# Kernel tuning notes

Measured on AMD Instinct MI355X. Metric: run time of the kernel, lower is better.

Reference implementation:

```python
import jax, jax.numpy as jnp
import numpy as np
from jax import lax

# flat indices of the 8 'donut' taps in a 3x3 kernel (center position 4 stays zero),
# matching torch.nonzero row-major ordering of the mask
_DONUT_IDX = jnp.array([0, 1, 2, 3, 5, 6, 7, 8])

def _gelu(x):
    return jax.nn.gelu(x, approximate=False)  # torch nn.GELU default (erf)

def _conv(x, w, dil=1, pad=0):
    return lax.conv_general_dilated(x, w, (1, 1), [(pad, pad), (pad, pad)],
                                    rhs_dilation=(dil, dil),
                                    dimension_numbers=('NCHW', 'OIHW', 'NCHW'))

def _donut_conv(x, p, dil):
    # ParamConv_reg_variable_dilation with shuffle_true=0: scatter 8 params into a
    # 3x3 kernel (zero center) and conv with rhs_dilation=dil, padding=dil ('same').
    O, I, _ = p.shape
    k = jnp.zeros((O, I, 9), p.dtype).at[:, :, _DONUT_IDX].set(p).reshape(O, I, 3, 3)
    return _conv(x, k, dil=dil, pad=dil)

def _resblock(x, w1, w2):
    # gelu(Sequential(conv3x3, gelu, conv3x3)(x) + x)
    return _gelu(_conv(_gelu(_conv(x, w1, pad=1)), w2, pad=1) + x)

def _avgpool2(x):
    N, C, H, W = x.shape
    return x.reshape(N, C, H // 2, 2, W // 2, 2).mean(axis=(3, 5))

def _upsample(x, scale, w):
    # nn.Upsample(scale, bilinear, align_corners=False) -> half-pixel bilinear resize
    N, C, H, W = x.shape
    if scale > 1:
        x = jax.image.resize(x, (N, C, H * scale, W * scale), method='bilinear')
    return _gelu(_conv(x, w))  # 1x1 conv + gelu

def _shine_fwd(input_image, conv0a_w, conv0b_w, first_p, cl10_w, cl2_w,
               dil_p, dilres_p, ups_w, out1_w, out2_w, last_w):
    # n_frames=5, center frame index 2; H,W divisible by 64 so no pad branch
    target = input_image[:, 2:3]
    feats = jnp.concatenate([input_image[:, :2], input_image[:, 3:]], axis=1)  # [N,4,H,W]
    target = _gelu(_conv(target, conv0b_w))            # 1x1 -> 48 ch
    feats = _gelu(_conv(feats, conv0a_w, pad=1))       # 3x3 -> 16 ch
    base = jnp.concatenate([target, feats], axis=1)    # 64 ch

    outs = [_gelu(_donut_conv(base, first_p, 1))]      # first_output (dil 1)
    base = _resblock(base, cl10_w[0, 0], cl10_w[0, 1])
    outs.append(_gelu(_donut_conv(base, dilres_p[0], 3)))  # dilated_convs_res[0]
    base = _resblock(base, cl2_w[0, 0], cl2_w[0, 1])

    dils = (5, 8, 10, 11)     # dilated_convs effective dilations (add_dilation=0)
    dilres = (3, 6, 8, 9)     # dilated_convs_res effective dilations
    for i in range(4):
        m = _gelu(_donut_conv(base, dil_p[i], dils[i]))
        outs.append(_upsample(m, 2 ** i, ups_w[i]))
        if i < 3:
            base = _avgpool2(base)
            base = _resblock(base, cl10_w[i + 1, 0], cl10_w[i + 1, 1])
            m = _gelu(_donut_conv(base, dilres_p[i + 1], dilres[i + 1]))
            outs.append(_upsample(m, 2 ** (i + 1), ups_w[i + 1]))
            base = _resblock(base, cl2_w[i + 1, 0], cl2_w[i + 1, 1])

    out = jnp.concatenate(outs, axis=1)                # 9*64 = 576 ch
    out = _gelu(_conv(out, out1_w))                    # 1x1 576->288
    out = _gelu(_conv(out, out2_w))                    # 1x1 288->64
    return _conv(out, last_w)                          # 1x1 64->1

def setup_inputs():
    key = jax.random.key(0)
    ks = jax.random.split(key, 12)
    s = 0.05
    F = 64
    return {
        'input_image': jax.random.normal(ks[0], (2, 5, 256, 256), jnp.float32),
        'conv0a_w': jax.random.normal(ks[1], (16, 4, 3, 3), jnp.float32) * s,
        'conv0b_w': jax.random.normal(ks[2], (48, 1, 1, 1), jnp.float32) * s,
        'first_p': jax.random.normal(ks[3], (F, F, 8), jnp.float32) * s,
        'cl10_w': jax.random.normal(ks[4], (4, 2, F, F, 3, 3), jnp.float32) * s,
        'cl2_w': jax.random.normal(ks[5], (4, 2, F, F, 3, 3), jnp.float32) * s,
        'dil_p': jax.random.normal(ks[6], (4, F, F, 8), jnp.float32) * s,
        'dilres_p': jax.random.normal(ks[7], (4, F, F, 8), jnp.float32) * s,
        'ups_w': jax.random.normal(ks[8], (4, F, F, 1, 1), jnp.float32) * s,
        'out1_w': jax.random.normal(ks[9], (288, 576, 1, 1), jnp.float32) * s,
        'out2_w': jax.random.normal(ks[10], (64, 288, 1, 1), jnp.float32) * s,
        'last_w': jax.random.normal(ks[11], (1, 64, 1, 1), jnp.float32) * s,
    }

def reference(input_image, conv0a_w, conv0b_w, first_p, cl10_w, cl2_w,
              dil_p, dilres_p, ups_w, out1_w, out2_w, last_w):
    return _shine_fwd(input_image, conv0a_w, conv0b_w, first_p, cl10_w, cl2_w,
                      dil_p, dilres_p, ups_w, out1_w, out2_w, last_w)
```

## Files before the change

### kernel.cpp

```cpp
#include <hip/hip_runtime.h>
#include <hip/hip_bf16.h>


#define HPX 65536
#define FCH 64

typedef __attribute__((ext_vector_type(8))) short  short8;
typedef __attribute__((ext_vector_type(4))) float  floatx4;

__device__ __forceinline__ float gelu_f(float x) {
  return 0.5f * x * (1.0f + erff(x * 0.70710678118654752440f));
}
__device__ __forceinline__ unsigned short f2bf(float x) {
  unsigned u = __float_as_uint(x);
  unsigned r = (u + 0x7FFFu + ((u >> 16) & 1u)) >> 16;
  return (unsigned short)r;
}
__device__ __forceinline__ float bf2f(unsigned short h) {
  return __uint_as_float(((unsigned)h) << 16);
}

__global__ __launch_bounds__(256) void conv0_nhwc_kernel(
    const float* __restrict__ img,
    const float* __restrict__ w0a,
    const float* __restrict__ w0b,
    unsigned short* __restrict__ ohi,
    unsigned short* __restrict__ olo)
{
  long t = (long)blockIdx.x * 256 + threadIdx.x;
  int c  = (int)(t & 63);
  int px = (int)((t >> 6) & (HPX - 1));
  int n  = (int)(t >> 22);
  const float* im = img + (long)n * 5 * HPX;
  float r;
  if (c < 48) {
    r = w0b[c] * im[2 * HPX + px];
  } else {
    int co = c - 48;
    int y = px >> 8, x = px & 255;
    r = 0.0f;
    const int map4[4] = {0, 1, 3, 4};
    #pragma unroll
    for (int fi = 0; fi < 4; fi++) {
      const float* imc = im + (long)map4[fi] * HPX;
      #pragma unroll
      for (int ky = 0; ky < 3; ky++) {
        int yy = y + ky - 1;
        #pragma unroll
        for (int kx = 0; kx < 3; kx++) {
          int xx = x + kx - 1;
          bool ok = ((unsigned)yy < 256u) && ((unsigned)xx < 256u);
          float v = ok ? imc[yy * 256 + xx] : 0.0f;
          r = fmaf(w0a[((co * 4 + fi) * 3 + ky) * 3 + kx], v, r);
        }
      }
    }
  }
  float v = gelu_f(r);
  unsigned short hb = f2bf(v);
  ohi[t] = hb;
  olo[t] = f2bf(v - bf2f(hb));
}

struct JobArr { int4 j[29]; };

__global__ __launch_bounds__(256) void pack_conv_kernel(
    const float* __restrict__ cl10, const float* __restrict__ cl2,
    const float* __restrict__ first_p, const float* __restrict__ dilres_p,
    const float* __restrict__ dil_p, const float* __restrict__ ups_w,
    unsigned short* __restrict__ packs, JobArr jobs)
{
  int4 jb = jobs.j[blockIdx.y];
  int ntaps = jb.z;
  int idx = blockIdx.x * 256 + threadIdx.x;
  if (idx >= ntaps * 8192) return;
  int j  = idx & 7;
  int l  = (idx >> 3) & 63;
  int s  = (idx >> 9) & 1;
  int nt = (idx >> 10) & 3;
  int kt = (idx >> 12) & 1;
  int tap = idx >> 13;
  int oc = nt * 16 + (l & 15);
  int ci = kt * 32 + (l >> 4) * 8 + j;
  const float* src;
  switch (jb.x) {
    case 0: src = cl10; break;
    case 1: src = cl2; break;
    case 2: src = first_p; break;
    case 3: src = dilres_p; break;
    case 4: src = dil_p; break;
    default: src = ups_w; break;
  }
  float w = src[jb.y + (oc * 64 + ci) * ntaps + tap];
  unsigned short hi = f2bf(w);
  unsigned short v = (s == 0) ? hi : f2bf(w - bf2f(hi));
  packs[jb.w + idx] = v;
}

__global__ __launch_bounds__(256) void pack_w1_kernel(
    const float* __restrict__ w1, unsigned short* __restrict__ w1p)
{
  int t = blockIdx.x * 256 + threadIdx.x;
  if (t >= 18 * 18 * 512) return;
  int j = t & 7, l = (t >> 3) & 63;
  int mt = (t >> 9) % 18, kt = (t >> 9) / 18;
  int oc = mt * 16 + (l & 15);
  int k  = kt * 32 + (l >> 4) * 8 + j;
  float w = w1[oc * 576 + k];
  unsigned short hi = f2bf(w);
  unsigned short lo = f2bf(w - bf2f(hi));
  long base = ((long)(kt * 18 + mt) * 2) * 512 + l * 8 + j;
  w1p[base] = hi;
  w1p[base + 512] = lo;
}
__global__ __launch_bounds__(256) void pack_w2_kernel(
    const float* __restrict__ w2, unsigned short* __restrict__ w2p)
{
  int t = blockIdx.x * 256 + threadIdx.x;
  if (t >= 9 * 4 * 512) return;
  int j = t & 7, l = (t >> 3) & 63;
  int ot = (t >> 9) % 4, kt = (t >> 9) / 4;
  int oc = ot * 16 + (l & 15);
  int k  = kt * 32 + (l >> 4) * 8 + j;
  float w = w2[oc * 288 + k];
  unsigned short hi = f2bf(w);
  unsigned short lo = f2bf(w - bf2f(hi));
  long base = ((long)(kt * 4 + ot) * 2) * 512 + l * 8 + j;
  w2p[base] = hi;
  w2p[base + 512] = lo;
}

template <int NTAPS, int MT, bool RESID, bool TO_CONCAT>
__global__ __launch_bounds__(256) void conv_pipe_kernel(
    const unsigned short* __restrict__ in_hi,
    const unsigned short* __restrict__ in_lo,
    const unsigned short* __restrict__ wp,
    const unsigned short* __restrict__ res_hi,
    const unsigned short* __restrict__ res_lo,
    unsigned short* __restrict__ out_hi,
    unsigned short* __restrict__ out_lo,
    int Hs, int logW, int dil, int ccol)
{
  __shared__ short8 wst[2][1024];
  const int tid  = threadIdx.x;
  const int lane = tid & 63;
  const int wave = tid >> 6;
  const int row  = lane & 15;
  const int g    = lane >> 4;
  const int n    = blockIdx.z;
  const int Ws   = 1 << logW;
  const int npx_in = Hs << logW;
  const int opx0 = blockIdx.x * (64 * MT) + wave * (16 * MT);

  const unsigned short* ihi = in_hi + (long)n * npx_in * 64;
  const unsigned short* ilo = in_lo + (long)n * npx_in * 64;
  const short8* wpv = (const short8*)wp;

  int ry[MT], rx[MT];
  #pragma unroll
  for (int mt = 0; mt < MT; mt++) {
    int p = opx0 + mt * 16 + row;
    ry[mt] = p >> logW;
    rx[mt] = p & (Ws - 1);
  }

  floatx4 acc[MT][4];
  #pragma unroll
  for (int mt = 0; mt < MT; mt++)
    #pragma unroll
    for (int nt = 0; nt < 4; nt++) acc[mt][nt] = (floatx4){0.f, 0.f, 0.f, 0.f};

  const short8 zz = {0, 0, 0, 0, 0, 0, 0, 0};
  short8 sreg[4];
  short8 ahA[MT][2], alA[MT][2], ahB[MT][2], alB[MT][2];

  auto stage_issue = [&](int t) {
    #pragma unroll
    for (int p = 0; p < 4; p++)
      sreg[p] = wpv[(long)t * 1024 + tid + p * 256];
  };
  auto stage_write = [&](int b) {
    #pragma unroll
    for (int p = 0; p < 4; p++)
      wst[b][tid + p * 256] = sreg[p];
  };
  auto a_load = [&](short8 (&ah)[MT][2], short8 (&al)[MT][2], int t) {
    const int kk  = (NTAPS == 9) ? t : (t < 4 ? t : t + 1);
    const int dyd = (kk / 3 - 1) * dil, dxd = (kk % 3 - 1) * dil;
    #pragma unroll
    for (int mt = 0; mt < MT; mt++) {
      int yy = ry[mt] + dyd, xx = rx[mt] + dxd;
      bool ok = ((unsigned)yy < (unsigned)Hs) && ((unsigned)xx < (unsigned)Ws);
      long base = ok ? (long)((yy << logW) + xx) * 64 : 0;
      #pragma unroll
      for (int kt = 0; kt < 2; kt++) {
        long a = base + kt * 32 + g * 8;
        short8 h = *(const short8*)(ihi + a);
        short8 l = *(const short8*)(ilo + a);
        ah[mt][kt] = ok ? h : zz;
        al[mt][kt] = ok ? l : zz;
      }
    }
  };
  auto compute = [&](int b, short8 (&ah)[MT][2], short8 (&al)[MT][2]) {
    #pragma unroll
    for (int kt = 0; kt < 2; kt++)
      #pragma unroll
      for (int nt = 0; nt < 4; nt++) {
        short8 bh = wst[b][(kt * 4 + nt) * 128 + lane];
        short8 bl = wst[b][(kt * 4 + nt) * 128 + 64 + lane];
        #pragma unroll
        for (int mt = 0; mt < MT; mt++) {
          acc[mt][nt] = __builtin_amdgcn_mfma_f32_16x16x32_bf16(ah[mt][kt], bh, acc[mt][nt], 0, 0, 0);
          acc[mt][nt] = __builtin_amdgcn_mfma_f32_16x16x32_bf16(ah[mt][kt], bl, acc[mt][nt], 0, 0, 0);
          acc[mt][nt] = __builtin_amdgcn_mfma_f32_16x16x32_bf16(al[mt][kt], bh, acc[mt][nt], 0, 0, 0);
        }
      }
  };

  stage_issue(0);
  a_load(ahA, alA, 0);
  stage_write(0);
  __syncthreads();

  #pragma unroll
  for (int tt = 0; tt < NTAPS; tt++) {
    const int b = tt & 1;
    if (tt + 1 < NTAPS) {
      stage_issue(tt + 1);
      if ((tt & 1) == 0) a_load(ahB, alB, tt + 1);
      else               a_load(ahA, alA, tt + 1);
    }
    if ((tt & 1) == 0) compute(b, ahA, alA);
    else               compute(b, ahB, alB);
    if (tt + 1 < NTAPS) {
      stage_write(b ^ 1);
      __syncthreads();
    }
  }

  #pragma unroll
  for (int mt = 0; mt < MT; mt++) {
    #pragma unroll
    for (int nt = 0; nt < 4; nt++) {
      #pragma unroll
      for (int r = 0; r < 4; r++) {
        int px = opx0 + mt * 16 + g * 4 + r;
        int oc = nt * 16 + row;
        float v = acc[mt][nt][r];
        if (RESID) {
          long ri = ((long)n * npx_in + px) * 64 + oc;
          v += bf2f(res_hi[ri]) + bf2f(res_lo[ri]);
        }
        v = gelu_f(v);
        if (TO_CONCAT) {
          out_hi[((long)n * HPX + px) * 576 + ccol + oc] = f2bf(v);
        } else {
          long oi = ((long)n * npx_in + px) * 64 + oc;
          unsigned short hb = f2bf(v);
          out_hi[oi] = hb;
          out_lo[oi] = f2bf(v - bf2f(hb));
        }
      }
    }
  }
}

template <int NTAPS, int MT, bool RESID, bool BILIN, bool TO_CONCAT>
__global__ __launch_bounds__(256) void conv_mfma_kernel(
    const unsigned short* __restrict__ in_hi,
    const unsigned short* __restrict__ in_lo,
    const unsigned short* __restrict__ wp,
    const unsigned short* __restrict__ res_hi,
    const unsigned short* __restrict__ res_lo,
    unsigned short* __restrict__ out_hi,
    unsigned short* __restrict__ out_lo,
    int Hs, int logW, int dil, int ccol)
{
  __shared__ short8 wst[1024];
  const int tid  = threadIdx.x;
  const int lane = threadIdx.x & 63;
  const int wave = threadIdx.x >> 6;
  const int row  = lane & 15;
  const int g    = lane >> 4;
  const int n    = blockIdx.z;
  const int npx_in = Hs << logW;
  const int opx0 = blockIdx.x * (64 * MT) + wave * (16 * MT);

  const unsigned short* ihi = in_hi + (long)n * npx_in * 64;
  const unsigned short* ilo = in_lo + (long)n * npx_in * 64;
  const short8* wpv = (const short8*)wp;

  int b00[MT], b01[MT], b10[MT], b11[MT];
  float bwx[MT], bwy[MT];
  #pragma unroll
  for (int mt = 0; mt < MT; mt++) {
    int p = opx0 + mt * 16 + row;
    int Y = p >> 8, X = p & 255;
    float sc = (float)Hs * (1.0f / 256.0f);
    float fy = ((float)Y + 0.5f) * sc - 0.5f;
    float fx = ((float)X + 0.5f) * sc - 0.5f;
    int y0 = (int)floorf(fy), x0 = (int)floorf(fx);
    bwy[mt] = fy - (float)y0; bwx[mt] = fx - (float)x0;
    int y0c = min(max(y0, 0), Hs - 1), y1c = min(max(y0 + 1, 0), Hs - 1);
    int x0c = min(max(x0, 0), Hs - 1), x1c = min(max(x0 + 1, 0), Hs - 1);
    b00[mt] = (y0c * Hs + x0c) * 64; b01[mt] = (y0c * Hs + x1c) * 64;
    b10[mt] = (y1c * Hs + x0c) * 64; b11[mt] = (y1c * Hs + x1c) * 64;
  }

  floatx4 acc[MT][4];
  #pragma unroll
  for (int mt = 0; mt < MT; mt++)
    #pragma unroll
    for (int nt = 0; nt < 4; nt++) acc[mt][nt] = (floatx4){0.f, 0.f, 0.f, 0.f};

  #pragma unroll
  for (int p = 0; p < 4; p++)
    wst[tid + p * 256] = wpv[tid + p * 256];
  __syncthreads();

  #pragma unroll
  for (int kt = 0; kt < 2; kt++) {
    const int ko = kt * 32 + g * 8;
    short8 ah[MT], al[MT];
    #pragma unroll
    for (int mt = 0; mt < MT; mt++) {
      short8 h00 = *(const short8*)(ihi + b00[mt] + ko);
      short8 l00 = *(const short8*)(ilo + b00[mt] + ko);
      short8 h01 = *(const short8*)(ihi + b01[mt] + ko);
      short8 l01 = *(const short8*)(ilo + b01[mt] + ko);
      short8 h10 = *(const short8*)(ihi + b10[mt] + ko);
      short8 l10 = *(const short8*)(ilo + b10[mt] + ko);
      short8 h11 = *(const short8*)(ihi + b11[mt] + ko);
      short8 l11 = *(const short8*)(ilo + b11[mt] + ko);
      short8 hh, ll;
      #pragma unroll
      for (int j = 0; j < 8; j++) {
        float v00 = bf2f((unsigned short)h00[j]) + bf2f((unsigned short)l00[j]);
        float v01 = bf2f((unsigned short)h01[j]) + bf2f((unsigned short)l01[j]);
        float v10 = bf2f((unsigned short)h10[j]) + bf2f((unsigned short)l10[j]);
        float v11 = bf2f((unsigned short)h11[j]) + bf2f((unsigned short)l11[j]);
        float v0 = v00 + bwx[mt] * (v01 - v00);
        float v1 = v10 + bwx[mt] * (v11 - v10);
        float v  = v0 + bwy[mt] * (v1 - v0);
        unsigned short hb = f2bf(v);
        hh[j] = (short)hb;
        ll[j] = (short)f2bf(v - bf2f(hb));
      }
      ah[mt] = hh; al[mt] = ll;
    }
    #pragma unroll
    for (int nt = 0; nt < 4; nt++) {
      short8 bh = wst[(kt * 4 + nt) * 2 * 64 + lane];
      short8 bl = wst[((kt * 4 + nt) * 2 + 1) * 64 + lane];
      #pragma unroll
      for (int mt = 0; mt < MT; mt++) {
        acc[mt][nt] = __builtin_amdgcn_mfma_f32_16x16x32_bf16(ah[mt], bh, acc[mt][nt], 0, 0, 0);
        acc[mt][nt] = __builtin_amdgcn_mfma_f32_16x16x32_bf16(ah[mt], bl, acc[mt][nt], 0, 0, 0);
        acc[mt][nt] = __builtin_amdgcn_mfma_f32_16x16x32_bf16(al[mt], bh, acc[mt][nt], 0, 0, 0);
      }
    }
  }

  #pragma unroll
  for (int mt = 0; mt < MT; mt++) {
    #pragma unroll
    for (int nt = 0; nt < 4; nt++) {
      #pragma unroll
      for (int r = 0; r < 4; r++) {
        int px = opx0 + mt * 16 + g * 4 + r;
        int oc = nt * 16 + row;
        float v = gelu_f(acc[mt][nt][r]);
        out_hi[((long)n * HPX + px) * 576 + ccol + oc] = f2bf(v);
      }
    }
  }
}

__global__ __launch_bounds__(256) void avgpool_nhwc_kernel(
    const unsigned short* __restrict__ ihi, const unsigned short* __restrict__ ilo,
    unsigned short* __restrict__ ohi, unsigned short* __restrict__ olo,
    int logWo)
{
  const int lognpo = 2 * logWo;
  long t = (long)blockIdx.x * 256 + threadIdx.x;
  int cg = (int)(t & 7);
  int p  = (int)((t >> 3) & ((1 << lognpo) - 1));
  int n  = (int)(t >> (3 + lognpo));
  int y = p >> logWo, x = p & ((1 << logWo) - 1);
  int Wi = 2 << logWo;
  long ib = ((long)n * (4 << lognpo) + (long)(2 * y) * Wi + 2 * x) * 64 + cg * 8;
  short8 h00 = *(const short8*)(ihi + ib);
  short8 h01 = *(const short8*)(ihi + ib + 64);
  short8 h10 = *(const short8*)(ihi + ib + (long)Wi * 64);
  short8 h11 = *(const short8*)(ihi + ib + (long)Wi * 64 + 64);
  short8 l00 = *(const short8*)(ilo + ib);
  short8 l01 = *(const short8*)(ilo + ib + 64);
  short8 l10 = *(const short8*)(ilo + ib + (long)Wi * 64);
  short8 l11 = *(const short8*)(ilo + ib + (long)Wi * 64 + 64);
  short8 oh, ol;
  #pragma unroll
  for (int j = 0; j < 8; j++) {
    float v = 0.25f * ((bf2f((unsigned short)h00[j]) + bf2f((unsigned short)l00[j])) +
                       (bf2f((unsigned short)h01[j]) + bf2f((unsigned short)l01[j])) +
                       (bf2f((unsigned short)h10[j]) + bf2f((unsigned short)l10[j])) +
                       (bf2f((unsigned short)h11[j]) + bf2f((unsigned short)l11[j])));
    unsigned short hb = f2bf(v);
    oh[j] = (short)hb;
    ol[j] = (short)f2bf(v - bf2f(hb));
  }
  long ob = (((long)n << lognpo) + p) * 64 + cg * 8;
  *(short8*)(ohi + ob) = oh;
  *(short8*)(olo + ob) = ol;
}

__global__ __launch_bounds__(256, 2) void head_mfma_kernel(
    const unsigned short* __restrict__ v,
    const unsigned short* __restrict__ w1p,
    const unsigned short* __restrict__ w2p,
    const float* __restrict__ w3,
    float* __restrict__ out)
{
  __shared__ unsigned short hs[128][296];
  const int lane = threadIdx.x & 63;
  const int wave = threadIdx.x >> 6;
  const int col  = lane & 15;
  const int g    = lane >> 4;
  const int n    = blockIdx.y;
  const int pxb  = blockIdx.x * 128;
  const unsigned short* vn = v + ((long)n * HPX + pxb + wave * 32) * 576;
  const short8* w1v = (const short8*)w1p;
  const short8* w2v = (const short8*)w2p;

  floatx4 acc[2][18];
  #pragma unroll
  for (int t = 0; t < 2; t++)
    #pragma unroll
    for (int mt = 0; mt < 18; mt++) acc[t][mt] = (floatx4){0.f, 0.f, 0.f, 0.f};

  for (int kt = 0; kt < 18; kt++) {
    const int ko = kt * 32 + g * 8;
    short8 a0 = *(const short8*)(vn + (long)col * 576 + ko);
    short8 a1 = *(const short8*)(vn + (long)(col + 16) * 576 + ko);
    #pragma unroll
    for (int mt = 0; mt < 18; mt++) {
      short8 bhi = w1v[((kt * 18 + mt) * 2 + 0) * 64 + lane];
      short8 blo = w1v[((kt * 18 + mt) * 2 + 1) * 64 + lane];
      acc[0][mt] = __builtin_amdgcn_mfma_f32_16x16x32_bf16(a0, bhi, acc[0][mt], 0, 0, 0);
      acc[0][mt] = __builtin_amdgcn_mfma_f32_16x16x32_bf16(a0, blo, acc[0][mt], 0, 0, 0);
      acc[1][mt] = __builtin_amdgcn_mfma_f32_16x16x32_bf16(a1, bhi, acc[1][mt], 0, 0, 0);
      acc[1][mt] = __builtin_amdgcn_mfma_f32_16x16x32_bf16(a1, blo, acc[1][mt], 0, 0, 0);
    }
  }
  #pragma unroll
  for (int t = 0; t < 2; t++)
    #pragma unroll
    for (int mt = 0; mt < 18; mt++)
      #pragma unroll
      for (int r = 0; r < 4; r++)
        hs[wave * 32 + t * 16 + g * 4 + r][mt * 16 + col] =
            f2bf(gelu_f(acc[t][mt][r]));
  __syncthreads();

  floatx4 acc2[2][4];
  #pragma unroll
  for (int t = 0; t < 2; t++)
    #pragma unroll
    for (int ot = 0; ot < 4; ot++) acc2[t][ot] = (floatx4){0.f, 0.f, 0.f, 0.f};

  for (int kt = 0; kt < 9; kt++) {
    short8 a[2];
    #pragma unroll
    for (int t = 0; t < 2; t++)
      a[t] = *(const short8*)&hs[wave * 32 + t * 16 + col][kt * 32 + g * 8];
    #pragma unroll
    for (int ot = 0; ot < 4; ot++) {
      short8 bhi = w2v[((kt * 4 + ot) * 2 + 0) * 64 + lane];
      short8 blo = w2v[((kt * 4 + ot) * 2 + 1) * 64 + lane];
      acc2[0][ot] = __builtin_amdgcn_mfma_f32_16x16x32_bf16(a[0], bhi, acc2[0][ot], 0, 0, 0);
      acc2[0][ot] = __builtin_amdgcn_mfma_f32_16x16x32_bf16(a[0], blo, acc2[0][ot], 0, 0, 0);
      acc2[1][ot] = __builtin_amdgcn_mfma_f32_16x16x32_bf16(a[1], bhi, acc2[1][ot], 0, 0, 0);
      acc2[1][ot] = __builtin_amdgcn_mfma_f32_16x16x32_bf16(a[1], blo, acc2[1][ot], 0, 0, 0);
    }
  }

  float w3r[4];
  #pragma unroll
  for (int ot = 0; ot < 4; ot++) w3r[ot] = w3[ot * 16 + col];
  #pragma unroll
  for (int t = 0; t < 2; t++) {
    float r[4] = {0.f, 0.f, 0.f, 0.f};
    #pragma unroll
    for (int ot = 0; ot < 4; ot++)
      #pragma unroll
      for (int rr = 0; rr < 4; rr++)
        r[rr] = fmaf(w3r[ot], gelu_f(acc2[t][ot][rr]), r[rr]);
    #pragma unroll
    for (int rr = 0; rr < 4; rr++) {
      r[rr] += __shfl_xor(r[rr], 1);
      r[rr] += __shfl_xor(r[rr], 2);
      r[rr] += __shfl_xor(r[rr], 4);
      r[rr] += __shfl_xor(r[rr], 8);
    }
    if (col == 0) {
      int px = pxb + wave * 32 + t * 16 + g * 4;
      #pragma unroll
      for (int rr = 0; rr < 4; rr++)
        out[(long)n * HPX + px + rr] = r[rr];
    }
  }
}

extern "C" void kernel_launch(void* const* d_in, const int* in_sizes, int n_in,
                              void* d_out, int out_size, void* d_ws, size_t ws_size,
                              hipStream_t stream) {
  const float* img      = (const float*)d_in[0];
  const float* w0a      = (const float*)d_in[1];
  const float* w0b      = (const float*)d_in[2];
  const float* first_p  = (const float*)d_in[3];
  const float* cl10     = (const float*)d_in[4];
  const float* cl2      = (const float*)d_in[5];
  const float* dil_p    = (const float*)d_in[6];
  const float* dilres_p = (const float*)d_in[7];
  const float* ups_w    = (const float*)d_in[8];
  const float* w1       = (const float*)d_in[9];
  const float* w2       = (const float*)d_in[10];
  const float* w3       = (const float*)d_in[11];

  const size_t CONCAT_B = 150994944ul;
  const size_t ACT_B    = 16777216ul;
  const size_t PACKS_B  = 3604480ul;
  const size_t W1P_B    = 663552ul;
  const size_t W2P_B    = 73728ul;
  const size_t NEED = CONCAT_B + 4 * ACT_B + PACKS_B + W1P_B + W2P_B;

  if (ws_size < NEED) {
    hipMemsetAsync(d_out, 0, (size_t)out_size * 4, stream);
    return;
  }

  char* wsb = (char*)d_ws;
  unsigned short* concat = (unsigned short*)wsb;
  unsigned short* Xhi = (unsigned short*)(wsb + CONCAT_B);
  unsigned short* Xlo = (unsigned short*)(wsb + CONCAT_B + ACT_B);
  unsigned short* Yhi = (unsigned short*)(wsb + CONCAT_B + 2 * ACT_B);
  unsigned short* Ylo = (unsigned short*)(wsb + CONCAT_B + 3 * ACT_B);
  unsigned short* packs = (unsigned short*)(wsb + CONCAT_B + 4 * ACT_B);
  unsigned short* w1p = (unsigned short*)(wsb + CONCAT_B + 4 * ACT_B + PACKS_B);
  unsigned short* w2p = (unsigned short*)(wsb + CONCAT_B + 4 * ACT_B + PACKS_B + W1P_B);

  auto off_cl10   = [](int c) { return (long)c * 73728; };
  auto off_cl2    = [](int c) { return 589824l + (long)c * 73728; };
  const long OFF_FIRST = 1179648;
  auto off_dilres = [](int k) { return 1245184l + (long)k * 65536; };
  auto off_dil    = [](int k) { return 1507328l + (long)k * 65536; };
  auto off_ups    = [](int k) { return 1769472l + (long)k * 8192; };

  JobArr jobs;
  for (int c = 0; c < 8; c++) jobs.j[c]     = {0, c * 36864, 9, (int)off_cl10(c)};
  for (int c = 0; c < 8; c++) jobs.j[8 + c] = {1, c * 36864, 9, (int)off_cl2(c)};
  jobs.j[16] = {2, 0, 8, (int)OFF_FIRST};
  for (int k = 0; k < 4; k++) jobs.j[17 + k] = {3, k * 32768, 8, (int)off_dilres(k)};
  for (int k = 0; k < 4; k++) jobs.j[21 + k] = {4, k * 32768, 8, (int)off_dil(k)};
  for (int k = 0; k < 4; k++) jobs.j[25 + k] = {5, k * 4096, 1, (int)off_ups(k)};
  pack_conv_kernel<<<dim3(288, 29), 256, 0, stream>>>(
      cl10, cl2, first_p, dilres_p, dil_p, ups_w, packs, jobs);
  pack_w1_kernel<<<(18 * 18 * 512 + 255) / 256, 256, 0, stream>>>(w1, w1p);
  pack_w2_kernel<<<(9 * 4 * 512 + 255) / 256, 256, 0, stream>>>(w2, w2p);

  conv0_nhwc_kernel<<<(2 * HPX * 64) / 256, 256, 0, stream>>>(img, w0a, w0b, Xhi, Xlo);

  auto conv9 = [&](const unsigned short* ih, const unsigned short* il, long wo,
                   unsigned short* oh, unsigned short* ol, int Hs, int logW) {
    int npx = Hs << logW;
    if (npx == HPX)
      conv_pipe_kernel<9, 2, false, false><<<dim3(npx / 128, 1, 2), 256, 0, stream>>>(
          ih, il, packs + wo, nullptr, nullptr, oh, ol, Hs, logW, 1, 0);
    else
      conv_pipe_kernel<9, 1, false, false><<<dim3(npx / 64, 1, 2), 256, 0, stream>>>(
          ih, il, packs + wo, nullptr, nullptr, oh, ol, Hs, logW, 1, 0);
  };
  auto conv9r = [&](const unsigned short* ih, const unsigned short* il, long wo,
                    unsigned short* rh, unsigned short* rl, int Hs, int logW) {
    int npx = Hs << logW;
    if (npx == HPX)
      conv_pipe_kernel<9, 2, true, false><<<dim3(npx / 128, 1, 2), 256, 0, stream>>>(
          ih, il, packs + wo, rh, rl, rh, rl, Hs, logW, 1, 0);
    else
      conv_pipe_kernel<9, 1, true, false><<<dim3(npx / 64, 1, 2), 256, 0, stream>>>(
          ih, il, packs + wo, rh, rl, rh, rl, Hs, logW, 1, 0);
  };
  auto donutC = [&](const unsigned short* ih, const unsigned short* il, long wo,
                    int dil, int ccol) {
    conv_pipe_kernel<8, 2, false, true><<<dim3(512, 1, 2), 256, 0, stream>>>(
        ih, il, packs + wo, nullptr, nullptr, concat, nullptr, 256, 8, dil, ccol);
  };
  auto donutA = [&](const unsigned short* ih, const unsigned short* il, long wo,
                    int dil, unsigned short* oh, unsigned short* ol, int Hs, int logW) {
    int npx = Hs << logW;
    if (npx == HPX)
      conv_pipe_kernel<8, 2, false, false><<<dim3(npx / 128, 1, 2), 256, 0, stream>>>(
          ih, il, packs + wo, nullptr, nullptr, oh, ol, Hs, logW, dil, 0);
    else
      conv_pipe_kernel<8, 1, false, false><<<dim3(npx / 64, 1, 2), 256, 0, stream>>>(
          ih, il, packs + wo, nullptr, nullptr, oh, ol, Hs, logW, dil, 0);
  };
  auto upsC = [&](const unsigned short* ih, const unsigned short* il, long wo,
                  int Hs, int logW, int ccol) {
    conv_mfma_kernel<1, 4, false, true, true><<<dim3(256, 1, 2), 256, 0, stream>>>(
        ih, il, packs + wo, nullptr, nullptr, concat, nullptr, Hs, logW, 1, ccol);
  };
  auto avgp = [&](const unsigned short* ih, const unsigned short* il,
                  unsigned short* oh, unsigned short* ol, int logWo) {
    long total = 2l * (1l << (2 * logWo)) * 8;
    avgpool_nhwc_kernel<<<(int)(total / 256), 256, 0, stream>>>(ih, il, oh, ol, logWo);
  };

  donutC(Xhi, Xlo, OFF_FIRST, 1, 0);
  conv9(Xhi, Xlo, off_cl10(0), Yhi, Ylo, 256, 8);
  conv9r(Yhi, Ylo, off_cl10(1), Xhi, Xlo, 256, 8);
  donutC(Xhi, Xlo, off_dilres(0), 3, 64);
  conv9(Xhi, Xlo, off_cl2(0), Yhi, Ylo, 256, 8);
  conv9r(Yhi, Ylo, off_cl2(1), Xhi, Xlo, 256, 8);

  donutA(Xhi, Xlo, off_dil(0), 5, Yhi, Ylo, 256, 8);
  upsC(Yhi, Ylo, off_ups(0), 256, 8, 128);
  avgp(Xhi, Xlo, Yhi, Ylo, 7);
  conv9(Yhi, Ylo, off_cl10(2), Xhi, Xlo, 128, 7);
  conv9r(Xhi, Xlo, off_cl10(3), Yhi, Ylo, 128, 7);
  donutA(Yhi, Ylo, off_dilres(1), 6, Xhi, Xlo, 128, 7);
  upsC(Xhi, Xlo, off_ups(1), 128, 7, 192);
  conv9(Yhi, Ylo, off_cl2(2), Xhi, Xlo, 128, 7);
  conv9r(Xhi, Xlo, off_cl2(3), Yhi, Ylo, 128, 7);

  donutA(Yhi, Ylo, off_dil(1), 8, Xhi, Xlo, 128, 7);
  upsC(Xhi, Xlo, off_ups(1), 128, 7, 256);
  avgp(Yhi, Ylo, Xhi, Xlo, 6);
  conv9(Xhi, Xlo, off_cl10(4), Yhi, Ylo, 64, 6);
  conv9r(Yhi, Ylo, off_cl10(5), Xhi, Xlo, 64, 6);
  donutA(Xhi, Xlo, off_dilres(2), 8, Yhi, Ylo, 64, 6);
  upsC(Yhi, Ylo, off_ups(2), 64, 6, 320);
  conv9(Xhi, Xlo, off_cl2(4), Yhi, Ylo, 64, 6);
  conv9r(Yhi, Ylo, off_cl2(5), Xhi, Xlo, 64, 6);

  donutA(Xhi, Xlo, off_dil(2), 10, Yhi, Ylo, 64, 6);
  upsC(Yhi, Ylo, off_ups(2), 64, 6, 384);
  avgp(Xhi, Xlo, Yhi, Ylo, 5);
  conv9(Yhi, Ylo, off_cl10(6), Xhi, Xlo, 32, 5);
  conv9r(Xhi, Xlo, off_cl10(7), Yhi, Ylo, 32, 5);
  donutA(Yhi, Ylo, off_dilres(3), 9, Xhi, Xlo, 32, 5);
  upsC(Xhi, Xlo, off_ups(3), 32, 5, 448);
  conv9(Yhi, Ylo, off_cl2(6), Xhi, Xlo, 32, 5);
  conv9r(Xhi, Xlo, off_cl2(7), Yhi, Ylo, 32, 5);

  donutA(Yhi, Ylo, off_dil(3), 11, Xhi, Xlo, 32, 5);
  upsC(Xhi, Xlo, off_ups(3), 32, 5, 512);

  head_mfma_kernel<<<dim3(512, 2), 256, 0, stream>>>(concat, w1p, w2p, w3,
                                                     (float*)d_out);
}
```

Baseline: 1.135 ms.

## Split head into staged out1/out2 GEMMs and coalesce conv epilogue stores via LDS

The fused head kernel, which held 18 accumulator tiles per wave and read w1 straight from global memory, is replaced by two kernels run over two pixel chunks. out1 stages each w1 k-slice in LDS, spreads the 288 output channels across waves, and writes gelu(h) to a scratch buffer. out2 then stages all of w2 in LDS and computes the 64-channel layer plus the final reduction. Separately, the conv and upsample epilogues now transpose results through per-wave LDS so global writes become 16-byte vector stores instead of scattered 2-byte stores. The intermediate h makes an extra round trip through global memory, and the scratch buffer reuses the X activation buffer.

```diff
diff --git a/kernel.cpp b/kernel.cpp
--- a/kernel.cpp
+++ b/kernel.cpp
@@ -4,6 +4,7 @@
 
 #define HPX 65536
 #define FCH 64
+#define CHPX 32768
 
 typedef __attribute__((ext_vector_type(8))) short  short8;
 typedef __attribute__((ext_vector_type(4))) float  floatx4;
@@ -141,7 +142,9 @@
     unsigned short* __restrict__ out_lo,
     int Hs, int logW, int dil, int ccol)
 {
+  constexpr int PL = TO_CONCAT ? 1 : 2;
   __shared__ short8 wst[2][1024];
+  __shared__ unsigned short tb[4][PL][16][76];
   const int tid  = threadIdx.x;
   const int lane = tid & 63;
   const int wave = tid >> 6;
@@ -241,6 +244,7 @@
 
   #pragma unroll
   for (int mt = 0; mt < MT; mt++) {
+    __builtin_amdgcn_wave_barrier();
     #pragma unroll
     for (int nt = 0; nt < 4; nt++) {
       #pragma unroll
@@ -253,31 +257,42 @@
           v += bf2f(res_hi[ri]) + bf2f(res_lo[ri]);
         }
         v = gelu_f(v);
+        unsigned short hb = f2bf(v);
+        tb[wave][0][g * 4 + r][oc] = hb;
+        if (!TO_CONCAT)
+          tb[wave][PL - 1][g * 4 + r][oc] = f2bf(v - bf2f(hb));
+      }
+    }
+    __builtin_amdgcn_wave_barrier();
+    const int pxb = opx0 + mt * 16;
+    const int pxl = lane >> 2;
+    #pragma unroll
+    for (int pl = 0; pl < PL; pl++) {
+      #pragma unroll
+      for (int it = 0; it < 2; it++) {
+        int ch = (lane & 3) + it * 4;
+        short8 v8 = *(const short8*)&tb[wave][pl][pxl][ch * 8];
         if (TO_CONCAT) {
-          out_hi[((long)n * HPX + px) * 576 + ccol + oc] = f2bf(v);
+          *(short8*)&out_hi[((long)n * HPX + pxb + pxl) * 576 + ccol + ch * 8] = v8;
         } else {
-          long oi = ((long)n * npx_in + px) * 64 + oc;
-          unsigned short hb = f2bf(v);
-          out_hi[oi] = hb;
-          out_lo[oi] = f2bf(v - bf2f(hb));
+          unsigned short* dst = pl ? out_lo : out_hi;
+          *(short8*)&dst[((long)n * npx_in + pxb + pxl) * 64 + ch * 8] = v8;
         }
       }
     }
   }
 }
 
-template <int NTAPS, int MT, bool RESID, bool BILIN, bool TO_CONCAT>
-__global__ __launch_bounds__(256) void conv_mfma_kernel(
+template <int MT>
+__global__ __launch_bounds__(256) void ups_mfma_kernel(
     const unsigned short* __restrict__ in_hi,
     const unsigned short* __restrict__ in_lo,
     const unsigned short* __restrict__ wp,
-    const unsigned short* __restrict__ res_hi,
-    const unsigned short* __restrict__ res_lo,
-    unsigned short* __restrict__ out_hi,
-    unsigned short* __restrict__ out_lo,
-    int Hs, int logW, int dil, int ccol)
+    unsigned short* __restrict__ outc,
+    int Hs, int logW, int ccol)
 {
   __shared__ short8 wst[1024];
+  __shared__ unsigned short tb[4][16][76];
   const int tid  = threadIdx.x;
   const int lane = threadIdx.x & 63;
   const int wave = threadIdx.x >> 6;
@@ -364,15 +379,20 @@
 
   #pragma unroll
   for (int mt = 0; mt < MT; mt++) {
-    #pragma unroll
-    for (int nt = 0; nt < 4; nt++) {
-      #pragma unroll
-      for (int r = 0; r < 4; r++) {
-        int px = opx0 + mt * 16 + g * 4 + r;
-        int oc = nt * 16 + row;
-        float v = gelu_f(acc[mt][nt][r]);
-        out_hi[((long)n * HPX + px) * 576 + ccol + oc] = f2bf(v);
-      }
+    __builtin_amdgcn_wave_barrier();
+    #pragma unroll
+    for (int nt = 0; nt < 4; nt++)
+      #pragma unroll
+      for (int r = 0; r < 4; r++)
+        tb[wave][g * 4 + r][nt * 16 + row] = f2bf(gelu_f(acc[mt][nt][r]));
+    __builtin_amdgcn_wave_barrier();
+    const int pxb = opx0 + mt * 16;
+    const int pxl = lane >> 2;
+    #pragma unroll
+    for (int it = 0; it < 2; it++) {
+      int ch = (lane & 3) + it * 4;
+      short8 v8 = *(const short8*)&tb[wave][pxl][ch * 8];
+      *(short8*)&outc[((long)n * HPX + pxb + pxl) * 576 + ccol + ch * 8] = v8;
     }
   }
 }
@@ -414,81 +434,130 @@
   *(short8*)(olo + ob) = ol;
 }
 
-__global__ __launch_bounds__(256, 2) void head_mfma_kernel(
+__global__ __launch_bounds__(256) void out1_gemm_kernel(
     const unsigned short* __restrict__ v,
     const unsigned short* __restrict__ w1p,
+    unsigned short* __restrict__ h,
+    int cpx)
+{
+  __shared__ short8 ws8[2400];
+  const int tid  = threadIdx.x;
+  const int lane = tid & 63;
+  const int wave = tid >> 6;
+  const int row  = lane & 15;
+  const int g    = lane >> 4;
+  const int n    = blockIdx.y;
+  const int px0  = cpx + blockIdx.x * 64;
+  const int mtb  = (wave < 2) ? wave * 5 : 10 + (wave - 2) * 4;
+  const int MTN  = (wave < 2) ? 5 : 4;
+  const short8* w1v = (const short8*)w1p;
+
+  floatx4 acc[4][5];
+  #pragma unroll
+  for (int t = 0; t < 4; t++)
+    #pragma unroll
+    for (int m = 0; m < 5; m++) acc[t][m] = (floatx4){0.f, 0.f, 0.f, 0.f};
+
+  for (int kt = 0; kt < 18; kt++) {
+    __syncthreads();
+    #pragma unroll
+    for (int p = 0; p < 9; p++)
+      ws8[tid + p * 256] = w1v[kt * 2304 + tid + p * 256];
+    __syncthreads();
+
+    short8 a[4];
+    #pragma unroll
+    for (int t = 0; t < 4; t++)
+      a[t] = *(const short8*)(v + ((long)n * HPX + px0 + t * 16 + row) * 576 +
+                              kt * 32 + g * 8);
+    #pragma unroll
+    for (int m = 0; m < 5; m++) {
+      if (m < MTN) {
+        short8 bh = ws8[((mtb + m) * 2 + 0) * 64 + lane];
+        short8 bl = ws8[((mtb + m) * 2 + 1) * 64 + lane];
+        #pragma unroll
+        for (int t = 0; t < 4; t++) {
+          acc[t][m] = __builtin_amdgcn_mfma_f32_16x16x32_bf16(a[t], bh, acc[t][m], 0, 0, 0);
+          acc[t][m] = __builtin_amdgcn_mfma_f32_16x16x32_bf16(a[t], bl, acc[t][m], 0, 0, 0);
+        }
+      }
+    }
+  }
+
+  __syncthreads();
+  unsigned short* hs2 = (unsigned short*)ws8;
+  #pragma unroll
+  for (int m = 0; m < 5; m++) {
+    if (m < MTN) {
+      #pragma unroll
+      for (int t = 0; t < 4; t++)
+        #pragma unroll
+        for (int r = 0; r < 4; r++)
+          hs2[(t * 16 + g * 4 + r) * 300 + (mtb + m) * 16 + row] =
+              f2bf(gelu_f(acc[t][m][r]));
+    }
+  }
+  __syncthreads();
+  #pragma unroll
+  for (int p = 0; p < 9; p++) {
+    int li = tid + p * 256;
+    int px = li / 36, c16 = li % 36;
+    short8 v8 = *(const short8*)&hs2[px * 300 + c16 * 8];
+    *(short8*)&h[((long)n * CHPX + (px0 - cpx) + px) * 288 + c16 * 8] = v8;
+  }
+}
+
+__global__ __launch_bounds__(256) void out2_gemm_kernel(
+    const unsigned short* __restrict__ h,
     const unsigned short* __restrict__ w2p,
     const float* __restrict__ w3,
-    float* __restrict__ out)
-{
-  __shared__ unsigned short hs[128][296];
-  const int lane = threadIdx.x & 63;
-  const int wave = threadIdx.x >> 6;
-  const int col  = lane & 15;
+    float* __restrict__ out,
+    int cpx)
+{
+  __shared__ short8 w2s[4608];
+  const int tid  = threadIdx.x;
+  const int lane = tid & 63;
+  const int wave = tid >> 6;
+  const int row  = lane & 15;
   const int g    = lane >> 4;
   const int n    = blockIdx.y;
-  const int pxb  = blockIdx.x * 128;
-  const unsigned short* vn = v + ((long)n * HPX + pxb + wave * 32) * 576;
-  const short8* w1v = (const short8*)w1p;
+  const int pxc  = blockIdx.x * 256 + wave * 64;
   const short8* w2v = (const short8*)w2p;
 
-  floatx4 acc[2][18];
-  #pragma unroll
-  for (int t = 0; t < 2; t++)
-    #pragma unroll
-    for (int mt = 0; mt < 18; mt++) acc[t][mt] = (floatx4){0.f, 0.f, 0.f, 0.f};
-
-  for (int kt = 0; kt < 18; kt++) {
-    const int ko = kt * 32 + g * 8;
-    short8 a0 = *(const short8*)(vn + (long)col * 576 + ko);
-    short8 a1 = *(const short8*)(vn + (long)(col + 16) * 576 + ko);
-    #pragma unroll
-    for (int mt = 0; mt < 18; mt++) {
-      short8 bhi = w1v[((kt * 18 + mt) * 2 + 0) * 64 + lane];
-      short8 blo = w1v[((kt * 18 + mt) * 2 + 1) * 64 + lane];
-      acc[0][mt] = __builtin_amdgcn_mfma_f32_16x16x32_bf16(a0, bhi, acc[0][mt], 0, 0, 0);
-      acc[0][mt] = __builtin_amdgcn_mfma_f32_16x16x32_bf16(a0, blo, acc[0][mt], 0, 0, 0);
-      acc[1][mt] = __builtin_amdgcn_mfma_f32_16x16x32_bf16(a1, bhi, acc[1][mt], 0, 0, 0);
-      acc[1][mt] = __builtin_amdgcn_mfma_f32_16x16x32_bf16(a1, blo, acc[1][mt], 0, 0, 0);
-    }
-  }
-  #pragma unroll
-  for (int t = 0; t < 2; t++)
-    #pragma unroll
-    for (int mt = 0; mt < 18; mt++)
-      #pragma unroll
-      for (int r = 0; r < 4; r++)
-        hs[wave * 32 + t * 16 + g * 4 + r][mt * 16 + col] =
-            f2bf(gelu_f(acc[t][mt][r]));
+  #pragma unroll
+  for (int p = 0; p < 18; p++)
+    w2s[tid + p * 256] = w2v[tid + p * 256];
   __syncthreads();
 
-  floatx4 acc2[2][4];
-  #pragma unroll
-  for (int t = 0; t < 2; t++)
+  floatx4 acc2[4][4];
+  #pragma unroll
+  for (int t = 0; t < 4; t++)
     #pragma unroll
     for (int ot = 0; ot < 4; ot++) acc2[t][ot] = (floatx4){0.f, 0.f, 0.f, 0.f};
 
   for (int kt = 0; kt < 9; kt++) {
-    short8 a[2];
-    #pragma unroll
-    for (int t = 0; t < 2; t++)
-      a[t] = *(const short8*)&hs[wave * 32 + t * 16 + col][kt * 32 + g * 8];
+    short8 a[4];
+    #pragma unroll
+    for (int t = 0; t < 4; t++)
+      a[t] = *(const short8*)&h[((long)n * CHPX + pxc + t * 16 + row) * 288 +
+                                kt * 32 + g * 8];
     #pragma unroll
     for (int ot = 0; ot < 4; ot++) {
-      short8 bhi = w2v[((kt * 4 + ot) * 2 + 0) * 64 + lane];
-      short8 blo = w2v[((kt * 4 + ot) * 2 + 1) * 64 + lane];
-      acc2[0][ot] = __builtin_amdgcn_mfma_f32_16x16x32_bf16(a[0], bhi, acc2[0][ot], 0, 0, 0);
-      acc2[0][ot] = __builtin_amdgcn_mfma_f32_16x16x32_bf16(a[0], blo, acc2[0][ot], 0, 0, 0);
-      acc2[1][ot] = __builtin_amdgcn_mfma_f32_16x16x32_bf16(a[1], bhi, acc2[1][ot], 0, 0, 0);
-      acc2[1][ot] = __builtin_amdgcn_mfma_f32_16x16x32_bf16(a[1], blo, acc2[1][ot], 0, 0, 0);
+      short8 bh = w2s[((kt * 4 + ot) * 2 + 0) * 64 + lane];
+      short8 bl = w2s[((kt * 4 + ot) * 2 + 1) * 64 + lane];
+      #pragma unroll
+      for (int t = 0; t < 4; t++) {
+        acc2[t][ot] = __builtin_amdgcn_mfma_f32_16x16x32_bf16(a[t], bh, acc2[t][ot], 0, 0, 0);
+        acc2[t][ot] = __builtin_amdgcn_mfma_f32_16x16x32_bf16(a[t], bl, acc2[t][ot], 0, 0, 0);
+      }
     }
   }
 
   float w3r[4];
   #pragma unroll
-  for (int ot = 0; ot < 4; ot++) w3r[ot] = w3[ot * 16 + col];
-  #pragma unroll
-  for (int t = 0; t < 2; t++) {
+  for (int ot = 0; ot < 4; ot++) w3r[ot] = w3[ot * 16 + row];
+  #pragma unroll
+  for (int t = 0; t < 4; t++) {
     float r[4] = {0.f, 0.f, 0.f, 0.f};
     #pragma unroll
     for (int ot = 0; ot < 4; ot++)
@@ -502,8 +571,8 @@
       r[rr] += __shfl_xor(r[rr], 4);
       r[rr] += __shfl_xor(r[rr], 8);
     }
-    if (col == 0) {
-      int px = pxb + wave * 32 + t * 16 + g * 4;
+    if (row == 0) {
+      int px = cpx + pxc + t * 16 + g * 4;
       #pragma unroll
       for (int rr = 0; rr < 4; rr++)
         out[(long)n * HPX + px + rr] = r[rr];
@@ -548,6 +617,7 @@
   unsigned short* packs = (unsigned short*)(wsb + CONCAT_B + 4 * ACT_B);
   unsigned short* w1p = (unsigned short*)(wsb + CONCAT_B + 4 * ACT_B + PACKS_B);
   unsigned short* w2p = (unsigned short*)(wsb + CONCAT_B + 4 * ACT_B + PACKS_B + W1P_B);
+  unsigned short* hbuf = Xhi;
 
   auto off_cl10   = [](int c) { return (long)c * 73728; };
   auto off_cl2    = [](int c) { return 589824l + (long)c * 73728; };
@@ -607,8 +677,8 @@
   };
   auto upsC = [&](const unsigned short* ih, const unsigned short* il, long wo,
                   int Hs, int logW, int ccol) {
-    conv_mfma_kernel<1, 4, false, true, true><<<dim3(256, 1, 2), 256, 0, stream>>>(
-        ih, il, packs + wo, nullptr, nullptr, concat, nullptr, Hs, logW, 1, ccol);
+    ups_mfma_kernel<4><<<dim3(256, 1, 2), 256, 0, stream>>>(
+        ih, il, packs + wo, concat, Hs, logW, ccol);
   };
   auto avgp = [&](const unsigned short* ih, const unsigned short* il,
                   unsigned short* oh, unsigned short* ol, int logWo) {
@@ -656,6 +726,10 @@
   donutA(Yhi, Ylo, off_dil(3), 11, Xhi, Xlo, 32, 5);
   upsC(Xhi, Xlo, off_ups(3), 32, 5, 512);
 
-  head_mfma_kernel<<<dim3(512, 2), 256, 0, stream>>>(concat, w1p, w2p, w3,
-                                                     (float*)d_out);
-}
+  for (int c = 0; c < 2; c++) {
+    out1_gemm_kernel<<<dim3(CHPX / 64, 2), 256, 0, stream>>>(
+        concat, w1p, hbuf, c * CHPX);
+    out2_gemm_kernel<<<dim3(CHPX / 256, 2), 256, 0, stream>>>(
+        hbuf, w2p, w3, (float*)d_out, c * CHPX);
+  }
+}
```

After: 1.090 ms. -3.9%, faster.
